# Optimization experiments

Hardware: AMD Instinct MI355X
Metric: run time of the kernel (lower is better)

## Reference

```python
import jax, jax.numpy as jnp
import numpy as np

# Static multi-scale feature map shapes (H_l, W_l)
SHAPES = ((112, 112), (56, 56), (28, 28))
D_MODEL, D_HEAD, N_HEADS, N_LEVELS, N_POINTS = 256, 64, 6, 3, 9


def setup_inputs() -> dict:
    key = jax.random.key(0)
    ks = jax.random.split(key, 14)
    N, Lq = 4, 2048
    Lin = sum(h * w for h, w in SHAPES)  # 16464
    s = 0.02  # weight init scale
    return {
        "tgt": jax.random.normal(ks[0], (N, Lq, D_MODEL), jnp.float32),
        "src": jax.random.normal(ks[1], (N, Lin, D_MODEL), jnp.float32),
        "query_pos": jax.random.normal(ks[2], (N, Lq, D_MODEL), jnp.float32),
        "reference_points": jax.random.uniform(ks[3], (N, Lq, N_LEVELS, 2), jnp.float32),
        "src_spatial_shapes": jnp.array(SHAPES, jnp.int32),
        "level_start_index": jnp.array([0, 112 * 112, 112 * 112 + 56 * 56], jnp.int32),
        "src_padding_mask": jnp.zeros((N, Lin), bool),
        "W_off": jax.random.normal(ks[4], (D_MODEL, N_HEADS * N_LEVELS * N_POINTS * 2), jnp.float32) * s,
        "b_off": jax.random.normal(ks[5], (N_HEADS * N_LEVELS * N_POINTS * 2,), jnp.float32) * 0.5,
        "W_attn": jax.random.normal(ks[6], (D_MODEL, N_HEADS * N_LEVELS * N_POINTS), jnp.float32) * s,
        "b_attn": jax.random.normal(ks[7], (N_HEADS * N_LEVELS * N_POINTS,), jnp.float32) * s,
        "W_val": jax.random.normal(ks[8], (D_MODEL, N_HEADS * D_HEAD), jnp.float32) * s,
        "b_val": jnp.zeros((N_HEADS * D_HEAD,), jnp.float32),
        "W_out": jax.random.normal(ks[9], (N_HEADS * D_HEAD, D_MODEL), jnp.float32) * s,
        "b_out": jnp.zeros((D_MODEL,), jnp.float32),
    }


def _bilinear_sample(v, loc, H_l, W_l):
    """v: (N, Hh, H_l*W_l, d) level values; loc: (N, Lq, Hh, P, 2) in [0,1].
    grid_sample(align_corners=False, padding_mode='zeros') equivalent.
    Returns (N, Hh, Lq, P, d)."""
    N, Hh, _, d = v.shape
    Lq, P = loc.shape[1], loc.shape[3]
    x = loc[..., 0] * W_l - 0.5  # (N, Lq, Hh, P)
    y = loc[..., 1] * H_l - 0.5
    x0 = jnp.floor(x)
    y0 = jnp.floor(y)
    wx1 = x - x0
    wy1 = y - y0
    wx0 = 1.0 - wx1
    wy0 = 1.0 - wy1
    x0i = x0.astype(jnp.int32)
    y0i = y0.astype(jnp.int32)

    def gather(xi, yi, w):
        inb = (xi >= 0) & (xi < W_l) & (yi >= 0) & (yi < H_l)
        xc = jnp.clip(xi, 0, W_l - 1)
        yc = jnp.clip(yi, 0, H_l - 1)
        idx = (yc * W_l + xc).transpose(0, 2, 1, 3).reshape(N, Hh, Lq * P)
        g = jnp.take_along_axis(v, idx[..., None], axis=2)  # (N, Hh, Lq*P, d)
        w_eff = (w * inb).transpose(0, 2, 1, 3).reshape(N, Hh, Lq * P, 1)
        return g * w_eff

    out = (gather(x0i, y0i, wx0 * wy0)
           + gather(x0i + 1, y0i, wx1 * wy0)
           + gather(x0i, y0i + 1, wx0 * wy1)
           + gather(x0i + 1, y0i + 1, wx1 * wy1))
    return out.reshape(N, Hh, Lq, P, d)


def reference(tgt, src, query_pos, reference_points, src_spatial_shapes,
              level_start_index, src_padding_mask, W_off, b_off, W_attn, b_attn,
              W_val, b_val, W_out, b_out):
    N, Lq, _ = tgt.shape
    Hh, d, L, P = N_HEADS, D_HEAD, N_LEVELS, N_POINTS
    q = tgt + query_pos  # with_pos_embed

    value = src @ W_val + b_val
    value = jnp.where(src_padding_mask[..., None], 0.0, value)
    value = value.reshape(N, -1, Hh, d).transpose(0, 2, 1, 3)  # (N, Hh, Lin, d)

    off = (q @ W_off + b_off).reshape(N, Lq, Hh, L, P, 2)
    attn = jax.nn.softmax((q @ W_attn + b_attn).reshape(N, Lq, Hh, L * P), axis=-1)
    attn = attn.reshape(N, Lq, Hh, L, P)

    # offset_normalizer = (W_l, H_l); loc in normalized [0,1] coordinates
    norm = jnp.array([[w, h] for h, w in SHAPES], dtype=q.dtype)  # (L, 2)
    loc = reference_points[:, :, None, :, None, :] + off / norm[None, None, None, :, None, :]

    out = jnp.zeros((N, Hh, Lq, d), dtype=q.dtype)
    start = 0
    for l, (H_l, W_l) in enumerate(SHAPES):
        v_l = value[:, :, start:start + H_l * W_l]
        sampled = _bilinear_sample(v_l, loc[:, :, :, l], H_l, W_l)  # (N, Hh, Lq, P, d)
        out = out + jnp.einsum('nhqpd,nqhp->nhqd', sampled, attn[:, :, :, l])
        start += H_l * W_l

    out = out.transpose(0, 2, 1, 3).reshape(N, Lq, Hh * d)
    return out @ W_out + b_out  # dropout = identity in eval mode
```

## Files before the change

kernel.cpp:

```cpp
#include <hip/hip_runtime.h>
#include <math.h>

#define NB 4
#define LQ 2048
#define DM 256
#define HH 6
#define DH 64
#define LIN 16464
#define NOA 512
#define NVAL 384

typedef unsigned short ushort_t;
typedef unsigned int uint_t;
typedef __attribute__((ext_vector_type(8))) short s8v;
typedef __attribute__((ext_vector_type(4))) float f4v;

__device__ __forceinline__ ushort_t f2bf(float f) {
  union { float f; unsigned u; } v; v.f = f;
  unsigned r = v.u + 0x7fffu + ((v.u >> 16) & 1u);
  return (ushort_t)(r >> 16);
}

__device__ __forceinline__ uint_t cvtpk(float lo, float hi) {
  uint_t r;
  asm("v_cvt_pk_bf16_f32 %0, %1, %2" : "=v"(r) : "v"(lo), "v"(hi));
  return r;
}

typedef __attribute__((address_space(3))) char lds_char_t;
typedef const __attribute__((address_space(1))) char glb_char_t;
__device__ __forceinline__ void gload16(const void* g, void* l) {
  __builtin_amdgcn_global_load_lds((glb_char_t*)g, (lds_char_t*)l, 16, 0, 0);
}

__global__ __launch_bounds__(256)
void prep_k(const float4* __restrict__ tgt, const float4* __restrict__ qpos,
            ushort4* __restrict__ q_bf,
            const float* __restrict__ W_val, ushort_t* __restrict__ bt_val,
            const float* __restrict__ W_off, const float* __restrict__ W_attn,
            ushort_t* __restrict__ bt_oa,
            const float* __restrict__ W_out, ushort_t* __restrict__ bt_out,
            const float* __restrict__ b_off, const float* __restrict__ b_attn,
            float* __restrict__ bias_oa) {
  const int blk = blockIdx.x, tid = threadIdx.x;
  if (blk < 2048) {
    const int i = blk * 256 + tid;
    float4 x = tgt[i], y = qpos[i];
    ushort4 r;
    r.x = f2bf(x.x + y.x); r.y = f2bf(x.y + y.y);
    r.z = f2bf(x.z + y.z); r.w = f2bf(x.w + y.w);
    q_bf[i] = r;
  } else {
    const int i = (blk - 2048) * 256 + tid;
    if (i < 98304) {
      const int n = i >> 8, k = i & 255;
      bt_val[i] = f2bf(W_val[(size_t)k * 384 + n]);
    } else if (i < 229376) {
      const int j = i - 98304;
      const int n = j >> 8, k = j & 255;
      float v = 0.f;
      if (n < 324) v = W_off[(size_t)k * 324 + n];
      else if (n < 486) v = W_attn[(size_t)k * 162 + (n - 324)];
      bt_oa[j] = f2bf(v);
    } else if (i < 327680) {
      const int j = i - 229376;
      const int n = j / 384, k = j - n * 384;
      bt_out[j] = f2bf(W_out[(size_t)k * 256 + n]);
    } else {
      const int j = i - 327680;
      if (j < 512) bias_oa[j] = (j < 324) ? b_off[j] : (j < 486 ? b_attn[j - 324] : 0.f);
    }
  }
}

template <int NBX, int NBY, int CPX>
__global__ __launch_bounds__(256)
void mfma_gemm_vsrc_k(const float* __restrict__ Src, const ushort_t* __restrict__ Wt,
                      const float* __restrict__ bias, ushort_t* __restrict__ Cout) {
  __shared__ char lds[3][16384];
  const int bid = blockIdx.x;
  const int r = (bid & 7) * CPX + (bid >> 3);
  if (r >= NBX * NBY) return;
  const int bx = r / NBY, by = r - bx * NBY;
  const int bq = bx / 129;
  const int rb = (bx - bq * 129) * 128;
  const int n0 = by * 128;

  const int t = threadIdx.x;
  const int lane = t & 63, wid = t >> 6;
  const int wr = wid >> 1, wc = wid & 1;
  const int l15 = lane & 15, kg = lane >> 4;

  const int srow = lane >> 2;
  const int koct = (lane & 3) ^ ((lane >> 3) & 3);
  const int rsw = (l15 >> 1) & 3;
  const size_t WS0 = (size_t)(n0 + wid * 16 + srow) * DM + koct * 8;
  const size_t WS1 = WS0 + (size_t)64 * DM;

  const int ar = t >> 1, aj = t & 1;
  const int asw = ((ar & 15) >> 1) & 3;
  const int o0 = (2 * aj) ^ asw, o1 = (2 * aj + 1) ^ asw;
  const int arow_l = (rb + ar < LIN) ? (rb + ar) : (LIN - 1);
  const float* abase = Src + (size_t)(bq * LIN + arow_l) * DM;
  char* const aw0 = (char*)&lds[0][0];

  f4v acc[4][4];
#pragma unroll
  for (int i = 0; i < 4; ++i)
#pragma unroll
    for (int j = 0; j < 4; ++j) acc[i][j] = (f4v){0.f, 0.f, 0.f, 0.f};

  float4 ld[4];

#define ACT_LOAD(ks_)                                                    \
  { const int kb_ = (ks_) << 5;                                          \
    ld[0] = *(const float4*)(abase + kb_ + o0 * 8);                      \
    ld[1] = *(const float4*)(abase + kb_ + o0 * 8 + 4);                  \
    ld[2] = *(const float4*)(abase + kb_ + o1 * 8);                      \
    ld[3] = *(const float4*)(abase + kb_ + o1 * 8 + 4); }

#define ACT_WRITE(ks_)                                                  \
  { char* d_ = &lds[(ks_) % 3][8192] + ar * 64 + aj * 32;               \
    uint4 c0, c1;                                                       \
    c0.x = cvtpk(ld[0].x, ld[0].y); c0.y = cvtpk(ld[0].z, ld[0].w);     \
    c0.z = cvtpk(ld[1].x, ld[1].y); c0.w = cvtpk(ld[1].z, ld[1].w);     \
    c1.x = cvtpk(ld[2].x, ld[2].y); c1.y = cvtpk(ld[2].z, ld[2].w);     \
    c1.z = cvtpk(ld[3].x, ld[3].y); c1.w = cvtpk(ld[3].z, ld[3].w);     \
    *(uint4*)(d_) = c0;                                                 \
    *(uint4*)(d_ + 16) = c1; }

#define GLOADW(ks_)                                                     \
  { char* d_ = &lds[(ks_) % 3][0]; const int ko_ = (ks_) << 5;          \
    gload16(Wt + WS0 + ko_, d_ + wid * 1024);                           \
    gload16(Wt + WS1 + ko_, d_ + 4096 + wid * 1024); }

  ACT_LOAD(0);
  GLOADW(0);
  asm volatile("s_waitcnt vmcnt(2)" ::: "memory");
  ACT_WRITE(0);
  ACT_LOAD(1);
  GLOADW(1);
  asm volatile("s_waitcnt vmcnt(2)" ::: "memory");
  ACT_WRITE(1);

  const int nk = DM >> 5;
  for (int ks = 0; ks < nk; ++ks) {
    if (ks + 2 < nk) ACT_LOAD(ks + 2);
    if (ks == nk - 1) asm volatile("s_waitcnt vmcnt(0)" ::: "memory");
    asm volatile("s_waitcnt lgkmcnt(0)" ::: "memory");
    __builtin_amdgcn_s_barrier();
    asm volatile("" ::: "memory");
    if (ks + 2 < nk) GLOADW(ks + 2);

    const char* d = &lds[ks % 3][0];
    s8v av[4], bv[4];
#pragma unroll
    for (int mr = 0; mr < 4; ++mr)
      av[mr] = *(const s8v*)(d + (wr * 64 + mr * 16 + l15) * 64 + ((kg ^ rsw) << 4));
#pragma unroll
    for (int nr = 0; nr < 4; ++nr)
      bv[nr] = *(const s8v*)(d + 8192 + (wc * 64 + nr * 16 + l15) * 64 + ((kg ^ rsw) << 4));
#pragma unroll
    for (int mr = 0; mr < 4; ++mr)
#pragma unroll
      for (int nr = 0; nr < 4; ++nr)
        acc[mr][nr] = __builtin_amdgcn_mfma_f32_16x16x32_bf16(av[mr], bv[nr],
                                                              acc[mr][nr], 0, 0, 0);

    if (ks + 2 < nk) {
      asm volatile("s_waitcnt vmcnt(2)" ::: "memory");
      ACT_WRITE(ks + 2);
    }
  }
#undef ACT_LOAD
#undef ACT_WRITE
#undef GLOADW

#pragma unroll
  for (int mr = 0; mr < 4; ++mr) {
    const int ch = n0 + wr * 64 + mr * 16 + kg * 4;
    const int h = ch >> 6, dd = ch & 63;
    const float4 b4 = *(const float4*)(bias + ch);
    ushort_t* obase = Cout + (size_t)(bq * HH + h) * LIN * DH + dd;
#pragma unroll
    for (int nr = 0; nr < 4; ++nr) {
      const int ii = rb + wc * 64 + nr * 16 + l15;
      if (ii < LIN) {
        ushort4 o;
        o.x = f2bf(acc[mr][nr][0] + b4.x);
        o.y = f2bf(acc[mr][nr][1] + b4.y);
        o.z = f2bf(acc[mr][nr][2] + b4.z);
        o.w = f2bf(acc[mr][nr][3] + b4.w);
        *(ushort4*)(obase + (size_t)ii * DH) = o;
      }
    }
  }
  (void)aw0;
}

template <int NBX, int NBY, int CPX>
__global__ __launch_bounds__(256)
void mfma_gemm_k(const ushort_t* __restrict__ Act, const ushort_t* __restrict__ Wt,
                 const float* __restrict__ bias, float* __restrict__ Cout,
                 int N, int K) {
  __shared__ char lds[3][16384];
  const int bid = blockIdx.x;
  const int r = (bid & 7) * CPX + (bid >> 3);
  if (r >= NBX * NBY) return;
  const int bx = r / NBY, by = r - bx * NBY;
  const int m0 = bx * 128, n0 = by * 128;

  const int t = threadIdx.x;
  const int lane = t & 63, wid = t >> 6;
  const int wr = wid >> 1, wc = wid & 1;
  const int l15 = lane & 15, kg = lane >> 4;
  const int nk = K >> 5;

  const int srow = lane >> 2;
  const int koct = (lane & 3) ^ ((lane >> 3) & 3);
  const int rsw = (l15 >> 1) & 3;

  const size_t WA0 = (size_t)(n0 + wid * 16 + srow) * K + koct * 8;
  const size_t WA1 = WA0 + (size_t)64 * K;
  const size_t XB0 = (size_t)(m0 + wid * 16 + srow) * K + koct * 8;
  const size_t XB1 = XB0 + (size_t)64 * K;

  f4v acc[4][4];
#pragma unroll
  for (int i = 0; i < 4; ++i)
#pragma unroll
    for (int j = 0; j < 4; ++j) acc[i][j] = (f4v){0.f, 0.f, 0.f, 0.f};

#define STAGE(ks_)                                                       \
  { char* d_ = &lds[(ks_) % 3][0]; const int ko_ = (ks_) << 5;           \
    gload16(Wt + WA0 + ko_,  d_ + wid * 1024);                           \
    gload16(Wt + WA1 + ko_,  d_ + 4096 + wid * 1024);                    \
    gload16(Act + XB0 + ko_, d_ + 8192 + wid * 1024);                    \
    gload16(Act + XB1 + ko_, d_ + 12288 + wid * 1024); }

  STAGE(0);
  STAGE(1);

  for (int ks = 0; ks < nk; ++ks) {
    if (ks + 1 < nk) {
      asm volatile("s_waitcnt vmcnt(4)" ::: "memory");
    } else {
      asm volatile("s_waitcnt vmcnt(0)" ::: "memory");
    }
    __builtin_amdgcn_s_barrier();
    asm volatile("" ::: "memory");
    if (ks + 2 < nk) STAGE(ks + 2);

    const char* d = &lds[ks % 3][0];
    s8v av[4], bv[4];
#pragma unroll
    for (int mr = 0; mr < 4; ++mr)
      av[mr] = *(const s8v*)(d + (wr * 64 + mr * 16 + l15) * 64 + ((kg ^ rsw) << 4));
#pragma unroll
    for (int nr = 0; nr < 4; ++nr)
      bv[nr] = *(const s8v*)(d + 8192 + (wc * 64 + nr * 16 + l15) * 64 + ((kg ^ rsw) << 4));
#pragma unroll
    for (int mr = 0; mr < 4; ++mr)
#pragma unroll
      for (int nr = 0; nr < 4; ++nr)
        acc[mr][nr] = __builtin_amdgcn_mfma_f32_16x16x32_bf16(av[mr], bv[nr],
                                                              acc[mr][nr], 0, 0, 0);
  }
#undef STAGE

#pragma unroll
  for (int mr = 0; mr < 4; ++mr) {
    const int ch = n0 + wr * 64 + mr * 16 + kg * 4;
    const float4 b4 = *(const float4*)(bias + ch);
#pragma unroll
    for (int nr = 0; nr < 4; ++nr) {
      const int qrow = m0 + wc * 64 + nr * 16 + l15;
      float4 v;
      v.x = acc[mr][nr][0] + b4.x;
      v.y = acc[mr][nr][1] + b4.y;
      v.z = acc[mr][nr][2] + b4.z;
      v.w = acc[mr][nr][3] + b4.w;
      *(float4*)(Cout + (size_t)qrow * N + ch) = v;
    }
  }
}

__global__ __launch_bounds__(256)
void deform_sample_k(const ushort_t* __restrict__ value,
                     const float* __restrict__ oa,
                     const float* __restrict__ refp,
                     uint_t* __restrict__ otmp) {
  __shared__ int4 sp[4][56];
  const int lane = threadIdx.x & 63, wv = threadIdx.x >> 6;
  const int wid = blockIdx.x * 4 + wv;
  const int s = wid >> 11;
  const int qq = wid & 2047;
  const int nb = s / HH, h = s - nb * HH;
  const int nq = nb * LQ + qq;

  float lg = -INFINITY;
  if (lane < 27) lg = oa[(size_t)nq * NOA + 324 + h * 27 + lane];
  float mx = lg;
#pragma unroll
  for (int m = 1; m < 64; m <<= 1) mx = fmaxf(mx, __shfl_xor(mx, m, 64));
  float e = (lane < 27) ? __expf(lg - mx) : 0.f;
  float ssum = e;
#pragma unroll
  for (int m = 1; m < 64; m <<= 1) ssum += __shfl_xor(ssum, m, 64);

  if (lane < 27) {
    const float aw = e / ssum;
    const int lvl = (lane >= 18) ? 2 : (lane >= 9 ? 1 : 0);
    const float Wf = (lvl == 0) ? 112.f : (lvl == 1 ? 56.f : 28.f);
    const int Wi = (lvl == 0) ? 112 : (lvl == 1 ? 56 : 28);
    const int base = (lvl == 0) ? 0 : (lvl == 1 ? 12544 : 15680);
    const float2 rp = *(const float2*)(refp + (size_t)nq * 6 + lvl * 2);
    const float2 of = *(const float2*)(oa + (size_t)nq * NOA + h * 54 + lane * 2);
    const float x = rp.x * Wf + of.x - 0.5f;
    const float y = rp.y * Wf + of.y - 0.5f;
    const float x0f = floorf(x), y0f = floorf(y);
    const float wx1 = x - x0f, wy1 = y - y0f;
    const float wx0 = 1.f - wx1, wy0 = 1.f - wy1;
    const int x0 = (int)x0f, y0 = (int)y0f;
    const int x1 = x0 + 1, y1 = y0 + 1;
    const bool bx0 = (x0 >= 0) & (x0 < Wi), bx1 = (x1 >= 0) & (x1 < Wi);
    const bool by0 = (y0 >= 0) & (y0 < Wi), by1 = (y1 >= 0) & (y1 < Wi);
    const int a00 = (bx0 & by0) ? ((base + y0 * Wi + x0) << 7) : 0;
    const int a01 = (bx1 & by0) ? ((base + y0 * Wi + x1) << 7) : 0;
    const int a10 = (bx0 & by1) ? ((base + y1 * Wi + x0) << 7) : 0;
    const int a11 = (bx1 & by1) ? ((base + y1 * Wi + x1) << 7) : 0;
    const float w00 = (bx0 & by0) ? aw * wx0 * wy0 : 0.f;
    const float w01 = (bx1 & by0) ? aw * wx1 * wy0 : 0.f;
    const float w10 = (bx0 & by1) ? aw * wx0 * wy1 : 0.f;
    const float w11 = (bx1 & by1) ? aw * wx1 * wy1 : 0.f;
    sp[wv][lane * 2 + 0] = make_int4(a00, __float_as_int(w00), a01, __float_as_int(w01));
    sp[wv][lane * 2 + 1] = make_int4(a10, __float_as_int(w10), a11, __float_as_int(w11));
  } else if (lane == 27) {
    sp[wv][54] = make_int4(0, 0, 0, 0);
    sp[wv][55] = make_int4(0, 0, 0, 0);
  }
  __syncthreads();

  const uint_t slice = (uint_t)__builtin_amdgcn_readfirstlane(s);
  const char* vbase = (const char*)value + (size_t)slice * (LIN * DH * 2);
  const int j4 = (lane & 31) * 4;
  const int half = lane >> 5;
  float a0 = 0.f, a1 = 0.f;
#pragma unroll 2
  for (int i = 0; i < 14; ++i) {
    const int pt = half * 14 + i;
    const int4 c01 = sp[wv][pt * 2];
    const int4 c23 = sp[wv][pt * 2 + 1];
    const uint_t u0 = *(const uint_t*)(vbase + (uint_t)(c01.x + j4));
    const uint_t u1 = *(const uint_t*)(vbase + (uint_t)(c01.z + j4));
    const uint_t u2 = *(const uint_t*)(vbase + (uint_t)(c23.x + j4));
    const uint_t u3 = *(const uint_t*)(vbase + (uint_t)(c23.z + j4));
    const float w0 = __int_as_float(c01.y), w1 = __int_as_float(c01.w);
    const float w2 = __int_as_float(c23.y), w3 = __int_as_float(c23.w);
    a0 += w0 * __uint_as_float(u0 << 16);
    a1 += w0 * __uint_as_float(u0 & 0xffff0000u);
    a0 += w1 * __uint_as_float(u1 << 16);
    a1 += w1 * __uint_as_float(u1 & 0xffff0000u);
    a0 += w2 * __uint_as_float(u2 << 16);
    a1 += w2 * __uint_as_float(u2 & 0xffff0000u);
    a0 += w3 * __uint_as_float(u3 << 16);
    a1 += w3 * __uint_as_float(u3 & 0xffff0000u);
  }
  a0 += __shfl_xor(a0, 32, 64);
  a1 += __shfl_xor(a1, 32, 64);
  if (lane < 32) {
    const uint_t packed = (uint_t)f2bf(a0) | ((uint_t)f2bf(a1) << 16);
    otmp[(size_t)nq * 192 + h * 32 + lane] = packed;
  }
}

extern "C" void kernel_launch(void* const* d_in, const int* in_sizes, int n_in,
                              void* d_out, int out_size, void* d_ws, size_t ws_size,
                              hipStream_t stream) {
  const float* tgt   = (const float*)d_in[0];
  const float* src   = (const float*)d_in[1];
  const float* qpos  = (const float*)d_in[2];
  const float* refp  = (const float*)d_in[3];
  const float* W_off  = (const float*)d_in[7];
  const float* b_off  = (const float*)d_in[8];
  const float* W_attn = (const float*)d_in[9];
  const float* b_attn = (const float*)d_in[10];
  const float* W_val  = (const float*)d_in[11];
  const float* b_val  = (const float*)d_in[12];
  const float* W_out  = (const float*)d_in[13];
  const float* b_out  = (const float*)d_in[14];

  char* ws = (char*)d_ws;
  ushort_t* val_bf  = (ushort_t*)(ws);
  float*    oa      = (float*)   (ws + 50577408);
  ushort_t* q_bf    = (ushort_t*)(ws + 67354624);
  uint_t*   otmp    = (uint_t*)  (ws + 71548928);
  ushort_t* bt_val  = (ushort_t*)(ws + 77840384);
  ushort_t* bt_oa   = (ushort_t*)(ws + 78036992);
  ushort_t* bt_out  = (ushort_t*)(ws + 78299136);
  float*    bias_oa = (float*)   (ws + 78495744);

  prep_k<<<3330, 256, 0, stream>>>((const float4*)tgt, (const float4*)qpos,
                                   (ushort4*)q_bf, W_val, bt_val,
                                   W_off, W_attn, bt_oa, W_out, bt_out,
                                   b_off, b_attn, bias_oa);

  mfma_gemm_vsrc_k<516, 3, 194><<<1552, 256, 0, stream>>>(
      src, bt_val, b_val, val_bf);
  mfma_gemm_k<64, 4, 32><<<256, 256, 0, stream>>>(
      q_bf, bt_oa, bias_oa, oa, NOA, DM);

  deform_sample_k<<<12288, 256, 0, stream>>>(val_bf, oa, refp, otmp);

  mfma_gemm_k<64, 2, 16><<<128, 256, 0, stream>>>(
      (const ushort_t*)otmp, bt_out, b_out, (float*)d_out, DM, NVAL);
}
```

Before: 112.3 us.

## Process two 128-row tiles per block in value projection GEMM

The value-projection GEMM now has each block compute two consecutive 128-row tiles of src, 256 rows in total, against the same 128-column weight slice. The pipelined loop runs 16 k-steps instead of 8 and writes out and resets the accumulators after the first tile. This halves the grid to 784 blocks, cutting per-block launch and prologue overhead and giving more steady-state pipelining per block. The cost is fewer blocks to fill the GPU's CUs and weight tiles that are still reloaded for each tile.

```diff
diff --git a/kernel.cpp b/kernel.cpp
--- a/kernel.cpp
+++ b/kernel.cpp
@@ -73,17 +73,17 @@
   }
 }
 
-template <int NBX, int NBY, int CPX>
+template <int CPX>
 __global__ __launch_bounds__(256)
 void mfma_gemm_vsrc_k(const float* __restrict__ Src, const ushort_t* __restrict__ Wt,
                       const float* __restrict__ bias, ushort_t* __restrict__ Cout) {
   __shared__ char lds[3][16384];
   const int bid = blockIdx.x;
   const int r = (bid & 7) * CPX + (bid >> 3);
-  if (r >= NBX * NBY) return;
-  const int bx = r / NBY, by = r - bx * NBY;
-  const int bq = bx / 129;
-  const int rb = (bx - bq * 129) * 128;
+  if (r >= 780) return;
+  const int bx = r / 3, by = r - bx * 3;
+  const int bq = bx / 65;
+  const int rb = (bx - bq * 65) * 256;
   const int n0 = by * 128;
 
   const int t = threadIdx.x;
@@ -97,12 +97,14 @@
   const size_t WS0 = (size_t)(n0 + wid * 16 + srow) * DM + koct * 8;
   const size_t WS1 = WS0 + (size_t)64 * DM;
 
-  const int ar = t >> 1, aj = t & 1;
-  const int asw = ((ar & 15) >> 1) & 3;
-  const int o0 = (2 * aj) ^ asw, o1 = (2 * aj + 1) ^ asw;
-  const int arow_l = (rb + ar < LIN) ? (rb + ar) : (LIN - 1);
-  const float* abase = Src + (size_t)(bq * LIN + arow_l) * DM;
-  char* const aw0 = (char*)&lds[0][0];
+  const int ar = t >> 2, sA = t & 3;
+  const int oA = sA ^ (((ar & 15) >> 1) & 3);
+  const int rA0 = rb + ar,        rA1 = rb + ar + 64;
+  const int rB0 = rb + 128 + ar,  rB1 = rb + 128 + ar + 64;
+  const float* p00 = Src + ((size_t)bq * LIN + (rA0 < LIN ? rA0 : LIN - 1)) * DM + oA * 8;
+  const float* p01 = Src + ((size_t)bq * LIN + (rA1 < LIN ? rA1 : LIN - 1)) * DM + oA * 8;
+  const float* p10 = Src + ((size_t)bq * LIN + (rB0 < LIN ? rB0 : LIN - 1)) * DM + oA * 8;
+  const float* p11 = Src + ((size_t)bq * LIN + (rB1 < LIN ? rB1 : LIN - 1)) * DM + oA * 8;
 
   f4v acc[4][4];
 #pragma unroll
@@ -112,27 +114,52 @@
 
   float4 ld[4];
 
-#define ACT_LOAD(ks_)                                                    \
-  { const int kb_ = (ks_) << 5;                                          \
-    ld[0] = *(const float4*)(abase + kb_ + o0 * 8);                      \
-    ld[1] = *(const float4*)(abase + kb_ + o0 * 8 + 4);                  \
-    ld[2] = *(const float4*)(abase + kb_ + o1 * 8);                      \
-    ld[3] = *(const float4*)(abase + kb_ + o1 * 8 + 4); }
-
-#define ACT_WRITE(ks_)                                                  \
-  { char* d_ = &lds[(ks_) % 3][8192] + ar * 64 + aj * 32;               \
+#define ACT_LOAD(g_)                                                     \
+  { const float* pa_ = ((g_) & 8) ? p10 : p00;                           \
+    const float* pb_ = ((g_) & 8) ? p11 : p01;                           \
+    const int kb_ = ((g_) & 7) << 5;                                     \
+    ld[0] = *(const float4*)(pa_ + kb_);                                 \
+    ld[1] = *(const float4*)(pa_ + kb_ + 4);                             \
+    ld[2] = *(const float4*)(pb_ + kb_);                                 \
+    ld[3] = *(const float4*)(pb_ + kb_ + 4); }
+
+#define ACT_WRITE(g_)                                                   \
+  { char* d_ = &lds[(g_) % 3][8192] + t * 16;                           \
     uint4 c0, c1;                                                       \
     c0.x = cvtpk(ld[0].x, ld[0].y); c0.y = cvtpk(ld[0].z, ld[0].w);     \
     c0.z = cvtpk(ld[1].x, ld[1].y); c0.w = cvtpk(ld[1].z, ld[1].w);     \
     c1.x = cvtpk(ld[2].x, ld[2].y); c1.y = cvtpk(ld[2].z, ld[2].w);     \
     c1.z = cvtpk(ld[3].x, ld[3].y); c1.w = cvtpk(ld[3].z, ld[3].w);     \
     *(uint4*)(d_) = c0;                                                 \
-    *(uint4*)(d_ + 16) = c1; }
-
-#define GLOADW(ks_)                                                     \
-  { char* d_ = &lds[(ks_) % 3][0]; const int ko_ = (ks_) << 5;          \
+    *(uint4*)(d_ + 4096) = c1; }
+
+#define GLOADW(g_)                                                      \
+  { char* d_ = &lds[(g_) % 3][0]; const int ko_ = ((g_) & 7) << 5;      \
     gload16(Wt + WS0 + ko_, d_ + wid * 1024);                           \
     gload16(Wt + WS1 + ko_, d_ + 4096 + wid * 1024); }
+
+#define FLUSH(tile_)                                                    \
+  {                                                                     \
+    _Pragma("unroll")                                                   \
+    for (int mr = 0; mr < 4; ++mr) {                                    \
+      const int ch = n0 + wr * 64 + mr * 16 + kg * 4;                   \
+      const int h = ch >> 6, dd = ch & 63;                              \
+      const float4 b4 = *(const float4*)(bias + ch);                    \
+      ushort_t* obase = Cout + (size_t)(bq * HH + h) * LIN * DH + dd;   \
+      _Pragma("unroll")                                                 \
+      for (int nr = 0; nr < 4; ++nr) {                                  \
+        const int ii = rb + (tile_) * 128 + wc * 64 + nr * 16 + l15;    \
+        if (ii < LIN) {                                                 \
+          ushort4 o;                                                    \
+          o.x = f2bf(acc[mr][nr][0] + b4.x);                            \
+          o.y = f2bf(acc[mr][nr][1] + b4.y);                            \
+          o.z = f2bf(acc[mr][nr][2] + b4.z);                            \
+          o.w = f2bf(acc[mr][nr][3] + b4.w);                            \
+          *(ushort4*)(obase + (size_t)ii * DH) = o;                     \
+        }                                                               \
+      }                                                                 \
+    }                                                                   \
+  }
 
   ACT_LOAD(0);
   GLOADW(0);
@@ -143,16 +170,15 @@
   asm volatile("s_waitcnt vmcnt(2)" ::: "memory");
   ACT_WRITE(1);
 
-  const int nk = DM >> 5;
-  for (int ks = 0; ks < nk; ++ks) {
-    if (ks + 2 < nk) ACT_LOAD(ks + 2);
-    if (ks == nk - 1) asm volatile("s_waitcnt vmcnt(0)" ::: "memory");
+  for (int gs = 0; gs < 16; ++gs) {
+    if (gs + 2 < 16) ACT_LOAD(gs + 2);
+    if (gs == 15) asm volatile("s_waitcnt vmcnt(0)" ::: "memory");
     asm volatile("s_waitcnt lgkmcnt(0)" ::: "memory");
     __builtin_amdgcn_s_barrier();
     asm volatile("" ::: "memory");
-    if (ks + 2 < nk) GLOADW(ks + 2);
-
-    const char* d = &lds[ks % 3][0];
+    if (gs + 2 < 16) GLOADW(gs + 2);
+
+    const char* d = &lds[gs % 3][0];
     s8v av[4], bv[4];
 #pragma unroll
     for (int mr = 0; mr < 4; ++mr)
@@ -167,35 +193,23 @@
         acc[mr][nr] = __builtin_amdgcn_mfma_f32_16x16x32_bf16(av[mr], bv[nr],
                                                               acc[mr][nr], 0, 0, 0);
 
-    if (ks + 2 < nk) {
+    if (gs + 2 < 16) {
       asm volatile("s_waitcnt vmcnt(2)" ::: "memory");
-      ACT_WRITE(ks + 2);
+      ACT_WRITE(gs + 2);
     }
-  }
+    if (gs == 7) {
+      FLUSH(0);
+#pragma unroll
+      for (int i = 0; i < 4; ++i)
+#pragma unroll
+        for (int j = 0; j < 4; ++j) acc[i][j] = (f4v){0.f, 0.f, 0.f, 0.f};
+    }
+  }
+  FLUSH(1);
 #undef ACT_LOAD
 #undef ACT_WRITE
 #undef GLOADW
-
-#pragma unroll
-  for (int mr = 0; mr < 4; ++mr) {
-    const int ch = n0 + wr * 64 + mr * 16 + kg * 4;
-    const int h = ch >> 6, dd = ch & 63;
-    const float4 b4 = *(const float4*)(bias + ch);
-    ushort_t* obase = Cout + (size_t)(bq * HH + h) * LIN * DH + dd;
-#pragma unroll
-    for (int nr = 0; nr < 4; ++nr) {
-      const int ii = rb + wc * 64 + nr * 16 + l15;
-      if (ii < LIN) {
-        ushort4 o;
-        o.x = f2bf(acc[mr][nr][0] + b4.x);
-        o.y = f2bf(acc[mr][nr][1] + b4.y);
-        o.z = f2bf(acc[mr][nr][2] + b4.z);
-        o.w = f2bf(acc[mr][nr][3] + b4.w);
-        *(ushort4*)(obase + (size_t)ii * DH) = o;
-      }
-    }
-  }
-  (void)aw0;
+#undef FLUSH
 }
 
 template <int NBX, int NBY, int CPX>
@@ -405,8 +419,7 @@
                                    W_off, W_attn, bt_oa, W_out, bt_out,
                                    b_off, b_attn, bias_oa);
 
-  mfma_gemm_vsrc_k<516, 3, 194><<<1552, 256, 0, stream>>>(
-      src, bt_val, b_val, val_bf);
+  mfma_gemm_vsrc_k<98><<<784, 256, 0, stream>>>(src, bt_val, b_val, val_bf);
   mfma_gemm_k<64, 4, 32><<<256, 256, 0, stream>>>(
       q_bf, bt_oa, bias_oa, oa, NOA, DM);
 
```

After: 115.2 us. +2.6%, slower.

## Restructure value projection GEMM into small 64-row tiles with register-resident weights

Applied to the files above, without the earlier changes.

Replaces the 128x128 pipelined value-projection GEMM with a kernel in which each block handles 64 flattened source rows by 128 output channels. Each wave holds its 32x256 weight slice in registers, and the full K=256 activation tile is staged into LDS once, so the K-loop needs no barriers. Rows are flattened across the batch, so no tile is padded. The change trades more blocks, with each row's activations reloaded by three blocks, and higher register pressure for simpler synchronization and better load balance.

```diff
diff --git a/kernel.cpp b/kernel.cpp
--- a/kernel.cpp
+++ b/kernel.cpp
@@ -73,129 +73,87 @@
   }
 }
 
-template <int NBX, int NBY, int CPX>
 __global__ __launch_bounds__(256)
 void mfma_gemm_vsrc_k(const float* __restrict__ Src, const ushort_t* __restrict__ Wt,
                       const float* __restrict__ bias, ushort_t* __restrict__ Cout) {
-  __shared__ char lds[3][16384];
+  __shared__ char alds[8][4096];
   const int bid = blockIdx.x;
-  const int r = (bid & 7) * CPX + (bid >> 3);
-  if (r >= NBX * NBY) return;
-  const int bx = r / NBY, by = r - bx * NBY;
-  const int bq = bx / 129;
-  const int rb = (bx - bq * 129) * 128;
-  const int n0 = by * 128;
+  const int chunk = bid / 3, cc = bid - chunk * 3;
+  const int g0 = chunk * 64;
 
   const int t = threadIdx.x;
-  const int lane = t & 63, wid = t >> 6;
-  const int wr = wid >> 1, wc = wid & 1;
+  const int lane = t & 63, w = t >> 6;
   const int l15 = lane & 15, kg = lane >> 4;
-
-  const int srow = lane >> 2;
-  const int koct = (lane & 3) ^ ((lane >> 3) & 3);
   const int rsw = (l15 >> 1) & 3;
-  const size_t WS0 = (size_t)(n0 + wid * 16 + srow) * DM + koct * 8;
-  const size_t WS1 = WS0 + (size_t)64 * DM;
-
-  const int ar = t >> 1, aj = t & 1;
-  const int asw = ((ar & 15) >> 1) & 3;
-  const int o0 = (2 * aj) ^ asw, o1 = (2 * aj + 1) ^ asw;
-  const int arow_l = (rb + ar < LIN) ? (rb + ar) : (LIN - 1);
-  const float* abase = Src + (size_t)(bq * LIN + arow_l) * DM;
-  char* const aw0 = (char*)&lds[0][0];
-
-  f4v acc[4][4];
-#pragma unroll
-  for (int i = 0; i < 4; ++i)
+
+  const int tr = t >> 2, sA = t & 3;
+  const int oA = sA ^ (((tr & 15) >> 1) & 3);
+  const float* pa = Src + (size_t)(g0 + tr) * DM + oA * 8;
+
+  float4 lf[16];
+#pragma unroll
+  for (int ks = 0; ks < 8; ++ks) {
+    lf[2 * ks]     = *(const float4*)(pa + ks * 32);
+    lf[2 * ks + 1] = *(const float4*)(pa + ks * 32 + 4);
+  }
+
+  const ushort_t* wp = Wt + (size_t)(cc * 128 + w * 32 + l15) * DM + kg * 8;
+  s8v wv[2][8];
+#pragma unroll
+  for (int mr = 0; mr < 2; ++mr)
+#pragma unroll
+    for (int ks = 0; ks < 8; ++ks)
+      wv[mr][ks] = *(const s8v*)(wp + mr * 16 * DM + ks * 32);
+
+#pragma unroll
+  for (int ks = 0; ks < 8; ++ks) {
+    uint4 c;
+    c.x = cvtpk(lf[2 * ks].x, lf[2 * ks].y);
+    c.y = cvtpk(lf[2 * ks].z, lf[2 * ks].w);
+    c.z = cvtpk(lf[2 * ks + 1].x, lf[2 * ks + 1].y);
+    c.w = cvtpk(lf[2 * ks + 1].z, lf[2 * ks + 1].w);
+    *(uint4*)(&alds[ks][t * 16]) = c;
+  }
+  __syncthreads();
+
+  f4v acc[2][4];
+#pragma unroll
+  for (int i = 0; i < 2; ++i)
 #pragma unroll
     for (int j = 0; j < 4; ++j) acc[i][j] = (f4v){0.f, 0.f, 0.f, 0.f};
 
-  float4 ld[4];
-
-#define ACT_LOAD(ks_)                                                    \
-  { const int kb_ = (ks_) << 5;                                          \
-    ld[0] = *(const float4*)(abase + kb_ + o0 * 8);                      \
-    ld[1] = *(const float4*)(abase + kb_ + o0 * 8 + 4);                  \
-    ld[2] = *(const float4*)(abase + kb_ + o1 * 8);                      \
-    ld[3] = *(const float4*)(abase + kb_ + o1 * 8 + 4); }
-
-#define ACT_WRITE(ks_)                                                  \
-  { char* d_ = &lds[(ks_) % 3][8192] + ar * 64 + aj * 32;               \
-    uint4 c0, c1;                                                       \
-    c0.x = cvtpk(ld[0].x, ld[0].y); c0.y = cvtpk(ld[0].z, ld[0].w);     \
-    c0.z = cvtpk(ld[1].x, ld[1].y); c0.w = cvtpk(ld[1].z, ld[1].w);     \
-    c1.x = cvtpk(ld[2].x, ld[2].y); c1.y = cvtpk(ld[2].z, ld[2].w);     \
-    c1.z = cvtpk(ld[3].x, ld[3].y); c1.w = cvtpk(ld[3].z, ld[3].w);     \
-    *(uint4*)(d_) = c0;                                                 \
-    *(uint4*)(d_ + 16) = c1; }
-
-#define GLOADW(ks_)                                                     \
-  { char* d_ = &lds[(ks_) % 3][0]; const int ko_ = (ks_) << 5;          \
-    gload16(Wt + WS0 + ko_, d_ + wid * 1024);                           \
-    gload16(Wt + WS1 + ko_, d_ + 4096 + wid * 1024); }
-
-  ACT_LOAD(0);
-  GLOADW(0);
-  asm volatile("s_waitcnt vmcnt(2)" ::: "memory");
-  ACT_WRITE(0);
-  ACT_LOAD(1);
-  GLOADW(1);
-  asm volatile("s_waitcnt vmcnt(2)" ::: "memory");
-  ACT_WRITE(1);
-
-  const int nk = DM >> 5;
-  for (int ks = 0; ks < nk; ++ks) {
-    if (ks + 2 < nk) ACT_LOAD(ks + 2);
-    if (ks == nk - 1) asm volatile("s_waitcnt vmcnt(0)" ::: "memory");
-    asm volatile("s_waitcnt lgkmcnt(0)" ::: "memory");
-    __builtin_amdgcn_s_barrier();
-    asm volatile("" ::: "memory");
-    if (ks + 2 < nk) GLOADW(ks + 2);
-
-    const char* d = &lds[ks % 3][0];
-    s8v av[4], bv[4];
-#pragma unroll
-    for (int mr = 0; mr < 4; ++mr)
-      av[mr] = *(const s8v*)(d + (wr * 64 + mr * 16 + l15) * 64 + ((kg ^ rsw) << 4));
+#pragma unroll
+  for (int ks = 0; ks < 8; ++ks) {
+    s8v bv[4];
 #pragma unroll
     for (int nr = 0; nr < 4; ++nr)
-      bv[nr] = *(const s8v*)(d + 8192 + (wc * 64 + nr * 16 + l15) * 64 + ((kg ^ rsw) << 4));
-#pragma unroll
-    for (int mr = 0; mr < 4; ++mr)
+      bv[nr] = *(const s8v*)(&alds[ks][(nr * 16 + l15) * 64 + ((kg ^ rsw) << 4)]);
+#pragma unroll
+    for (int mr = 0; mr < 2; ++mr)
 #pragma unroll
       for (int nr = 0; nr < 4; ++nr)
-        acc[mr][nr] = __builtin_amdgcn_mfma_f32_16x16x32_bf16(av[mr], bv[nr],
+        acc[mr][nr] = __builtin_amdgcn_mfma_f32_16x16x32_bf16(wv[mr][ks], bv[nr],
                                                               acc[mr][nr], 0, 0, 0);
-
-    if (ks + 2 < nk) {
-      asm volatile("s_waitcnt vmcnt(2)" ::: "memory");
-      ACT_WRITE(ks + 2);
-    }
-  }
-#undef ACT_LOAD
-#undef ACT_WRITE
-#undef GLOADW
-
-#pragma unroll
-  for (int mr = 0; mr < 4; ++mr) {
-    const int ch = n0 + wr * 64 + mr * 16 + kg * 4;
+  }
+
+#pragma unroll
+  for (int mr = 0; mr < 2; ++mr) {
+    const int ch = cc * 128 + w * 32 + mr * 16 + kg * 4;
     const int h = ch >> 6, dd = ch & 63;
     const float4 b4 = *(const float4*)(bias + ch);
-    ushort_t* obase = Cout + (size_t)(bq * HH + h) * LIN * DH + dd;
 #pragma unroll
     for (int nr = 0; nr < 4; ++nr) {
-      const int ii = rb + wc * 64 + nr * 16 + l15;
-      if (ii < LIN) {
-        ushort4 o;
-        o.x = f2bf(acc[mr][nr][0] + b4.x);
-        o.y = f2bf(acc[mr][nr][1] + b4.y);
-        o.z = f2bf(acc[mr][nr][2] + b4.z);
-        o.w = f2bf(acc[mr][nr][3] + b4.w);
-        *(ushort4*)(obase + (size_t)ii * DH) = o;
-      }
+      const int g = g0 + nr * 16 + l15;
+      const int bq = g / LIN;
+      const int ii = g - bq * LIN;
+      ushort4 o;
+      o.x = f2bf(acc[mr][nr][0] + b4.x);
+      o.y = f2bf(acc[mr][nr][1] + b4.y);
+      o.z = f2bf(acc[mr][nr][2] + b4.z);
+      o.w = f2bf(acc[mr][nr][3] + b4.w);
+      *(ushort4*)(Cout + ((size_t)(bq * HH + h) * LIN + ii) * DH + dd) = o;
     }
   }
-  (void)aw0;
 }
 
 template <int NBX, int NBY, int CPX>
@@ -405,8 +363,7 @@
                                    W_off, W_attn, bt_oa, W_out, bt_out,
                                    b_off, b_attn, bias_oa);
 
-  mfma_gemm_vsrc_k<516, 3, 194><<<1552, 256, 0, stream>>>(
-      src, bt_val, b_val, val_bf);
+  mfma_gemm_vsrc_k<<<3087, 256, 0, stream>>>(src, bt_val, b_val, val_bf);
   mfma_gemm_k<64, 4, 32><<<256, 256, 0, stream>>>(
       q_bf, bt_oa, bias_oa, oa, NOA, DM);
 
```

Measured after the change: 125.7 us. 12.0% more time.
